# Optimization experiments

Hardware: AMD Instinct MI355X
Metric: run time of the kernel (lower is better)

## Reference

```python
import jax, jax.numpy as jnp
import numpy as np

# Hardcoded output spatial dims from the original call() (EEG: 62 channels x 375 timesteps)
H, W = 62, 375
N = 16            # batch size
P = H * W         # 23250 patch positions (x_1 dim of cal_val)
KFLAT = 1 * 5 * 25  # flattened kernel size = prod(output_dimension)
F = 64            # number of filters


def setup_inputs() -> dict:
    key = jax.random.key(0)
    k1, k2, k3 = jax.random.split(key, 3)
    x = jax.random.normal(k1, (N, P, KFLAT), dtype=jnp.float32)            # cal_val
    encoding_vector = jax.random.normal(k2, (P, KFLAT), dtype=jnp.float32)
    w = jax.random.normal(k3, (1, 5, 25, F), dtype=jnp.float32) * 0.05      # learned kernel
    return {"x": x, "encoding_vector": encoding_vector, "w": w}


def reference(x, encoding_vector, w):
    n, p, k = x.shape
    f = w.shape[-1]
    # build() flattens each filter: Kernel[j] = w[:, :, :, j].reshape(-1)  -> [F, kflat]
    kernel = jnp.moveaxis(w, 3, 0).reshape(f, k)
    # Original per-filter loop computes sum_k (kernel[f,k] + enc[p,k]) * x[n,p,k]
    # without materializing the tiled [N, P, kflat] kernel tensor:
    # out[f,n,p] = <kernel[f], x[n,p]> + <enc[p], x[n,p]>
    out_fnp = jnp.einsum('fk,npk->fnp', kernel, x) \
        + jnp.einsum('pk,npk->np', encoding_vector, x)[None, :, :]
    # Faithful final reshape of stacked [F, N, P] tensor into [N, F, H, W]
    return out_fnp.reshape(n, f, H, W)
```

## Files before the change

kernel.cpp:

```cpp
#include <hip/hip_runtime.h>


#define P_    23250
#define K_    125
#define F_    64
#define N_    16
#define M_TOT 372000
#define NPT   364
#define NWG   (NPT * N_)
#define CPX   (NWG / 8)
#define TSTR  68

typedef __bf16 bf16;
typedef __bf16 bf16x4 __attribute__((ext_vector_type(4)));
typedef __bf16 bf16x8 __attribute__((ext_vector_type(8)));
typedef float  f32x4  __attribute__((ext_vector_type(4)));
typedef float  f32x4u __attribute__((ext_vector_type(4), aligned(4)));

__global__ __launch_bounds__(256, 1)
void prep_wfrag(const float* __restrict__ w, bf16* __restrict__ wfrag)
{
    const int tid = threadIdx.x;
    const int f  = ((tid >> 6) << 4) | (tid & 15);
    const int kg = (tid >> 4) & 3;
    #pragma unroll
    for (int ks = 0; ks < 4; ++ks) {
        bf16x8 fr;
        #pragma unroll
        for (int j = 0; j < 8; ++j) {
            const int k = ks * 32 + kg * 8 + j;
            fr[j] = (bf16)((k < K_) ? w[k * F_ + f] : 0.0f);
        }
        *(bf16x8*)(wfrag + tid * 32 + ks * 8) = fr;
    }
}

__global__ __launch_bounds__(256, 4)
void eegconv_kernel(const float* __restrict__ x,
                    const float* __restrict__ enc,
                    const bf16* __restrict__ wfrag,
                    float* __restrict__ out)
{
    __shared__ __attribute__((aligned(16))) char raw[F_ * TSTR * 4];
    __shared__ __attribute__((aligned(16))) float srow[64];

    const int tid  = threadIdx.x;
    const int lane = tid & 63;
    const int wv   = tid >> 6;
    const int fl   = lane & 15;
    const int kg   = lane >> 4;

    const int wgid  = (blockIdx.x & 7) * CPX + (blockIdx.x >> 3);
    const int ptile = wgid >> 4;
    const int n     = wgid & 15;
    const int p0    = ptile * 64;

    bf16x8 kf[4];
    {
        const bf16x8* wf = (const bf16x8*)(wfrag + tid * 32);
        #pragma unroll
        for (int ks = 0; ks < 4; ++ks) kf[ks] = wf[ks];
    }

    bf16* xt = (bf16*)raw;
    {
        const int row = tid >> 2;
        const int t4  = tid & 3;
        const int p   = p0 + row;
        const int pe  = (p < P_) ? p : 0;
        const float* xr = x   + (size_t)(n * P_ + pe) * K_;
        const float* er = enc + (size_t)pe * K_;
        char* lbase = (char*)xt + row * 256;
        const int sw = (row & 7) << 4;
        float part = 0.0f;

        #pragma unroll
        for (int u = 0; u < 8; ++u) {
            const int c = u * 4 + t4;
            f32x4 xv, ev;
            if (c < 31) {
                xv = (f32x4)*(const f32x4u*)(xr + c * 4);
                ev = (f32x4)*(const f32x4u*)(er + c * 4);
            } else {
                xv = f32x4{xr[124], 0.f, 0.f, 0.f};
                ev = f32x4{er[124], 0.f, 0.f, 0.f};
            }
            part += ev.x * xv.x + ev.y * xv.y + ev.z * xv.z + ev.w * xv.w;
            bf16x4 bv;
            bv[0] = (bf16)xv.x; bv[1] = (bf16)xv.y; bv[2] = (bf16)xv.z; bv[3] = (bf16)xv.w;
            *(bf16x4*)(lbase + ((c * 8) ^ sw)) = bv;
        }
        part += __shfl_xor(part, 1);
        part += __shfl_xor(part, 2);
        if (t4 == 0) srow[row] = part;
    }
    __syncthreads();

    f32x4 acc[4];
    #pragma unroll
    for (int t = 0; t < 4; ++t) acc[t] = f32x4{0.f, 0.f, 0.f, 0.f};

    #pragma unroll
    for (int t = 0; t < 4; ++t) {
        const int il = t * 16 + fl;
        const char* rbase = (const char*)xt + il * 256;
        const int sw = (il & 7) << 4;
        #pragma unroll
        for (int ks = 0; ks < 4; ++ks) {
            const bf16x8 av = *(const bf16x8*)(rbase + ((ks * 64 + kg * 16) ^ sw));
            acc[t] = __builtin_amdgcn_mfma_f32_16x16x32_bf16(av, kf[ks], acc[t], 0, 0, 0);
        }
    }
    __syncthreads();

    float* tr = (float*)raw;
    {
        const int f = wv * 16 + fl;
        #pragma unroll
        for (int t = 0; t < 4; ++t) {
            const int i0 = t * 16 + kg * 4;
            *(f32x4*)(tr + f * TSTR + i0) = acc[t];
        }
    }
    __syncthreads();

    {
        const int m8 = tid & 7;
        const int fg = tid >> 3;
        const bool full = (p0 + 64 <= P_);
        #pragma unroll
        for (int pp = 0; pp < 2; ++pp) {
            const int f = pp * 32 + fg;
            const float* src = tr + f * TSTR;
            float* ob = out + (size_t)f * M_TOT + (size_t)n * P_ + p0;
            #pragma unroll
            for (int h = 0; h < 2; ++h) {
                const int ii = h * 32 + m8 * 4;
                f32x4 v  = *(const f32x4*)(src + ii);
                const f32x4 sv = *(const f32x4*)(srow + ii);
                v.x += sv.x; v.y += sv.y; v.z += sv.z; v.w += sv.w;
                if (full) {
                    *(f32x4u*)(ob + ii) = v;
                } else {
                    #pragma unroll
                    for (int e = 0; e < 4; ++e)
                        if (p0 + ii + e < P_) ob[ii + e] = v[e];
                }
            }
        }
    }
}

extern "C" void kernel_launch(void* const* d_in, const int* in_sizes, int n_in,
                              void* d_out, int out_size, void* d_ws, size_t ws_size,
                              hipStream_t stream)
{
    const float* x   = (const float*)d_in[0];
    const float* enc = (const float*)d_in[1];
    const float* w   = (const float*)d_in[2];
    float* out = (float*)d_out;
    bf16* wfrag = (bf16*)d_ws;
    prep_wfrag<<<1, 256, 0, stream>>>(w, wfrag);
    eegconv_kernel<<<NWG, 256, 0, stream>>>(x, enc, wfrag, out);
}
```

Before: 325.7 us.

## Process two batch items per workgroup, reuse encoding rows, store MFMA output directly

Each workgroup now handles two batch indices for one 64-position tile, so the encoding row is loaded once and reused for both dot products. The second batch's x loads are issued before the first batch's MFMA and stores, overlapping global loads with compute. The LDS transpose stage is removed and accumulators are written straight to global memory as 16-byte chunks, which drops a sync and the LDS round trip but gives a less coalesced store pattern. The grid is halved and register pressure goes up because of the held ev/xv arrays.

```diff
diff --git a/kernel.cpp b/kernel.cpp
--- a/kernel.cpp
+++ b/kernel.cpp
@@ -4,12 +4,10 @@
 #define P_    23250
 #define K_    125
 #define F_    64
-#define N_    16
 #define M_TOT 372000
 #define NPT   364
-#define NWG   (NPT * N_)
+#define NWG   (NPT * 8)
 #define CPX   (NWG / 8)
-#define TSTR  68
 
 typedef __bf16 bf16;
 typedef __bf16 bf16x4 __attribute__((ext_vector_type(4)));
@@ -41,8 +39,8 @@
                     const bf16* __restrict__ wfrag,
                     float* __restrict__ out)
 {
-    __shared__ __attribute__((aligned(16))) char raw[F_ * TSTR * 4];
-    __shared__ __attribute__((aligned(16))) float srow[64];
+    __shared__ __attribute__((aligned(16))) bf16  xt[2][64 * 128];
+    __shared__ __attribute__((aligned(16))) float srow[2][64];
 
     const int tid  = threadIdx.x;
     const int lane = tid & 63;
@@ -51,9 +49,10 @@
     const int kg   = lane >> 4;
 
     const int wgid  = (blockIdx.x & 7) * CPX + (blockIdx.x >> 3);
-    const int ptile = wgid >> 4;
-    const int n     = wgid & 15;
+    const int ptile = wgid >> 3;
+    const int npair = wgid & 7;
     const int p0    = ptile * 64;
+    const int n0    = npair * 2;
 
     bf16x8 kf[4];
     {
@@ -62,90 +61,138 @@
         for (int ks = 0; ks < 4; ++ks) kf[ks] = wf[ks];
     }
 
-    bf16* xt = (bf16*)raw;
-    {
-        const int row = tid >> 2;
-        const int t4  = tid & 3;
-        const int p   = p0 + row;
-        const int pe  = (p < P_) ? p : 0;
-        const float* xr = x   + (size_t)(n * P_ + pe) * K_;
-        const float* er = enc + (size_t)pe * K_;
-        char* lbase = (char*)xt + row * 256;
-        const int sw = (row & 7) << 4;
-        float part = 0.0f;
-
+    const int row = tid >> 2;
+    const int t4  = tid & 3;
+    const int p   = p0 + row;
+    const int pe  = (p < P_) ? p : (P_ - 1);
+    const float* er  = enc + (size_t)pe * K_;
+    const float* xr0 = x + (size_t)(n0 * P_ + pe) * K_;
+    const float* xr1 = x + (size_t)((n0 + 1) * P_ + pe) * K_;
+    char* lb0 = (char*)&xt[0][0] + row * 256;
+    char* lb1 = (char*)&xt[1][0] + row * 256;
+    const int sw = (row & 7) << 4;
+
+    f32x4 ev[8], xv[8];
+    #pragma unroll
+    for (int u = 0; u < 8; ++u) {
+        const int c = u * 4 + t4;
+        if (c < 31) ev[u] = (f32x4)*(const f32x4u*)(er + c * 4);
+        else        ev[u] = f32x4{er[124], 0.f, 0.f, 0.f};
+    }
+    #pragma unroll
+    for (int u = 0; u < 8; ++u) {
+        const int c = u * 4 + t4;
+        if (c < 31) xv[u] = (f32x4)*(const f32x4u*)(xr0 + c * 4);
+        else        xv[u] = f32x4{xr0[124], 0.f, 0.f, 0.f};
+    }
+    {
+        float part = 0.f;
         #pragma unroll
         for (int u = 0; u < 8; ++u) {
             const int c = u * 4 + t4;
-            f32x4 xv, ev;
-            if (c < 31) {
-                xv = (f32x4)*(const f32x4u*)(xr + c * 4);
-                ev = (f32x4)*(const f32x4u*)(er + c * 4);
-            } else {
-                xv = f32x4{xr[124], 0.f, 0.f, 0.f};
-                ev = f32x4{er[124], 0.f, 0.f, 0.f};
-            }
-            part += ev.x * xv.x + ev.y * xv.y + ev.z * xv.z + ev.w * xv.w;
+            part += ev[u].x * xv[u].x + ev[u].y * xv[u].y
+                  + ev[u].z * xv[u].z + ev[u].w * xv[u].w;
             bf16x4 bv;
-            bv[0] = (bf16)xv.x; bv[1] = (bf16)xv.y; bv[2] = (bf16)xv.z; bv[3] = (bf16)xv.w;
-            *(bf16x4*)(lbase + ((c * 8) ^ sw)) = bv;
+            bv[0] = (bf16)xv[u].x; bv[1] = (bf16)xv[u].y;
+            bv[2] = (bf16)xv[u].z; bv[3] = (bf16)xv[u].w;
+            *(bf16x4*)(lb0 + ((c * 8) ^ sw)) = bv;
         }
         part += __shfl_xor(part, 1);
         part += __shfl_xor(part, 2);
-        if (t4 == 0) srow[row] = part;
+        if (t4 == 0) srow[0][row] = part;
     }
     __syncthreads();
 
-    f32x4 acc[4];
-    #pragma unroll
-    for (int t = 0; t < 4; ++t) acc[t] = f32x4{0.f, 0.f, 0.f, 0.f};
-
-    #pragma unroll
-    for (int t = 0; t < 4; ++t) {
-        const int il = t * 16 + fl;
-        const char* rbase = (const char*)xt + il * 256;
-        const int sw = (il & 7) << 4;
-        #pragma unroll
-        for (int ks = 0; ks < 4; ++ks) {
-            const bf16x8 av = *(const bf16x8*)(rbase + ((ks * 64 + kg * 16) ^ sw));
-            acc[t] = __builtin_amdgcn_mfma_f32_16x16x32_bf16(av, kf[ks], acc[t], 0, 0, 0);
-        }
+    #pragma unroll
+    for (int u = 0; u < 8; ++u) {
+        const int c = u * 4 + t4;
+        if (c < 31) xv[u] = (f32x4)*(const f32x4u*)(xr1 + c * 4);
+        else        xv[u] = f32x4{xr1[124], 0.f, 0.f, 0.f};
+    }
+
+    const size_t fM   = (size_t)(wv * 16 + fl) * (size_t)M_TOT;
+    const bool   full = (p0 + 64 <= P_);
+
+    {
+        f32x4 acc[4];
+        #pragma unroll
+        for (int t = 0; t < 4; ++t) acc[t] = f32x4{0.f, 0.f, 0.f, 0.f};
+        #pragma unroll
+        for (int t = 0; t < 4; ++t) {
+            const int il = t * 16 + fl;
+            const char* rb = (const char*)&xt[0][0] + il * 256;
+            const int s2 = (il & 7) << 4;
+            #pragma unroll
+            for (int ks = 0; ks < 4; ++ks) {
+                const bf16x8 av = *(const bf16x8*)(rb + ((ks * 64 + kg * 16) ^ s2));
+                acc[t] = __builtin_amdgcn_mfma_f32_16x16x32_bf16(av, kf[ks], acc[t], 0, 0, 0);
+            }
+        }
+        float* ob = out + fM + (size_t)n0 * P_ + p0;
+        #pragma unroll
+        for (int t = 0; t < 4; ++t) {
+            const int i0 = t * 16 + kg * 4;
+            const f32x4 sv = *(const f32x4*)(&srow[0][i0]);
+            f32x4 v;
+            v.x = acc[t][0] + sv.x; v.y = acc[t][1] + sv.y;
+            v.z = acc[t][2] + sv.z; v.w = acc[t][3] + sv.w;
+            if (full) {
+                *(f32x4u*)(ob + i0) = v;
+            } else {
+                #pragma unroll
+                for (int e = 0; e < 4; ++e)
+                    if (p0 + i0 + e < P_) ob[i0 + e] = v[e];
+            }
+        }
+    }
+
+    {
+        float part = 0.f;
+        #pragma unroll
+        for (int u = 0; u < 8; ++u) {
+            const int c = u * 4 + t4;
+            part += ev[u].x * xv[u].x + ev[u].y * xv[u].y
+                  + ev[u].z * xv[u].z + ev[u].w * xv[u].w;
+            bf16x4 bv;
+            bv[0] = (bf16)xv[u].x; bv[1] = (bf16)xv[u].y;
+            bv[2] = (bf16)xv[u].z; bv[3] = (bf16)xv[u].w;
+            *(bf16x4*)(lb1 + ((c * 8) ^ sw)) = bv;
+        }
+        part += __shfl_xor(part, 1);
+        part += __shfl_xor(part, 2);
+        if (t4 == 0) srow[1][row] = part;
     }
     __syncthreads();
 
-    float* tr = (float*)raw;
-    {
-        const int f = wv * 16 + fl;
+    {
+        f32x4 acc[4];
+        #pragma unroll
+        for (int t = 0; t < 4; ++t) acc[t] = f32x4{0.f, 0.f, 0.f, 0.f};
+        #pragma unroll
+        for (int t = 0; t < 4; ++t) {
+            const int il = t * 16 + fl;
+            const char* rb = (const char*)&xt[1][0] + il * 256;
+            const int s2 = (il & 7) << 4;
+            #pragma unroll
+            for (int ks = 0; ks < 4; ++ks) {
+                const bf16x8 av = *(const bf16x8*)(rb + ((ks * 64 + kg * 16) ^ s2));
+                acc[t] = __builtin_amdgcn_mfma_f32_16x16x32_bf16(av, kf[ks], acc[t], 0, 0, 0);
+            }
+        }
+        float* ob = out + fM + (size_t)(n0 + 1) * P_ + p0;
         #pragma unroll
         for (int t = 0; t < 4; ++t) {
             const int i0 = t * 16 + kg * 4;
-            *(f32x4*)(tr + f * TSTR + i0) = acc[t];
-        }
-    }
-    __syncthreads();
-
-    {
-        const int m8 = tid & 7;
-        const int fg = tid >> 3;
-        const bool full = (p0 + 64 <= P_);
-        #pragma unroll
-        for (int pp = 0; pp < 2; ++pp) {
-            const int f = pp * 32 + fg;
-            const float* src = tr + f * TSTR;
-            float* ob = out + (size_t)f * M_TOT + (size_t)n * P_ + p0;
-            #pragma unroll
-            for (int h = 0; h < 2; ++h) {
-                const int ii = h * 32 + m8 * 4;
-                f32x4 v  = *(const f32x4*)(src + ii);
-                const f32x4 sv = *(const f32x4*)(srow + ii);
-                v.x += sv.x; v.y += sv.y; v.z += sv.z; v.w += sv.w;
-                if (full) {
-                    *(f32x4u*)(ob + ii) = v;
-                } else {
-                    #pragma unroll
-                    for (int e = 0; e < 4; ++e)
-                        if (p0 + ii + e < P_) ob[ii + e] = v[e];
-                }
+            const f32x4 sv = *(const f32x4*)(&srow[1][i0]);
+            f32x4 v;
+            v.x = acc[t][0] + sv.x; v.y = acc[t][1] + sv.y;
+            v.z = acc[t][2] + sv.z; v.w = acc[t][3] + sv.w;
+            if (full) {
+                *(f32x4u*)(ob + i0) = v;
+            } else {
+                #pragma unroll
+                for (int e = 0; e < 4; ++e)
+                    if (p0 + i0 + e < P_) ob[i0 + e] = v[e];
             }
         }
     }
```

Result: faster. 316.1 us (-3.0%).
